# Kernel optimization log

Hardware: AMD Instinct MI355X
Metric: run time of the kernel (lower is better)

## Reference

```python
import jax, jax.numpy as jnp
import numpy as np
import math

B, H, S, D = 2, 16, 2048, 64


def setup_inputs() -> dict:
    key = jax.random.key(0)
    kq, kk, kv = jax.random.split(key, 3)
    q = jax.random.normal(kq, (B, H, S, D), dtype=jnp.float32)
    k = jax.random.normal(kk, (B, H, S, D), dtype=jnp.float32)
    v = jax.random.normal(kv, (B, H, S, D), dtype=jnp.float32)
    # causal lower-triangular mask, broadcastable to [B, H, S, S]
    mask = jnp.tril(jnp.ones((S, S), dtype=jnp.int32))[None, None, :, :]
    return {"q": q, "k": k, "v": v, "mask": mask}


def reference(q, k, v, mask):
    d_tensor = q.shape[-1]
    # scores: [B, H, S, S] = q @ k^T / sqrt(d)
    scores = jnp.einsum("bhqd,bhkd->bhqk", q, k) / math.sqrt(d_tensor)
    scores = jnp.where(mask == 0, jnp.float32(-100000.0), scores)
    attn = jax.nn.softmax(scores, axis=-1)
    out = jnp.einsum("bhqk,bhkd->bhqd", attn, v)
    return (out, attn)
```

## Files before the change

### kernel.cpp

```cpp
#include <hip/hip_runtime.h>

#define S_LEN 2048
#define D_DIM 64
#define NBH   32
#define BQ    64
#define SCALE2 0.1803368801f
#define KST   72

typedef _Float16 half8 __attribute__((ext_vector_type(8)));
typedef _Float16 half4 __attribute__((ext_vector_type(4)));
typedef float    fx4   __attribute__((ext_vector_type(4)));

#define BAR() do {                                            \
    asm volatile("s_waitcnt lgkmcnt(0)" ::: "memory");        \
    __builtin_amdgcn_s_barrier();                             \
    asm volatile("" ::: "memory");                            \
} while (0)

__global__ __launch_bounds__(256, 3)
void attn_fused(const float* __restrict__ Q, const float* __restrict__ K,
                const float* __restrict__ V, float* __restrict__ Out,
                float* __restrict__ Attn) {
    const int bh  = blockIdx.x;
    const int qt  = (int)(gridDim.y - 1) - (int)blockIdx.y;
    const int q0  = qt * BQ;
    const int T   = qt + 1;

    const int tid  = threadIdx.x;
    const int lane = tid & 63;
    const int w    = tid >> 6;
    const int ln15 = lane & 15;
    const int quad = lane >> 4;

    __shared__ _Float16 smem[5 * 64 * KST];
    _Float16 (*kb0)[KST] = (_Float16 (*)[KST])&smem[0];
    _Float16 (*kb1)[KST] = (_Float16 (*)[KST])&smem[64 * KST];
    _Float16 (*vb0)[KST] = (_Float16 (*)[KST])&smem[2 * 64 * KST];
    _Float16 (*vb1)[KST] = (_Float16 (*)[KST])&smem[3 * 64 * KST];
    _Float16 (*pw)[KST]  = (_Float16 (*)[KST])&smem[4 * 64 * KST + w * 16 * KST];
    _Float16 (*q_s)[KST] = kb1;

    const float* Qb = Q + ((size_t)bh * S_LEN + q0) * D_DIM;
    const float* Kb = K + (size_t)bh * S_LEN * D_DIM;
    const float* Vb = V + (size_t)bh * S_LEN * D_DIM;

    const int sr  = tid >> 4;
    const int sc4 = tid & 15;
    const int vc4 = tid >> 4;
    const int vjg = tid & 15;

    const float4* ks0 = (const float4*)Kb;
    float4 kf0 = ks0[tid], kf1 = ks0[256 + tid], kf2 = ks0[512 + tid], kf3 = ks0[768 + tid];
    {
        const float4* src = (const float4*)Qb;
        #pragma unroll
        for (int u = 0; u < 4; ++u) {
            int i = u * 256 + tid;
            int r = i >> 4, c4 = i & 15;
            float4 f = src[i];
            half4 h = {(_Float16)(f.x * SCALE2), (_Float16)(f.y * SCALE2),
                       (_Float16)(f.z * SCALE2), (_Float16)(f.w * SCALE2)};
            *(half4*)&q_s[r][c4 * 4] = h;
        }
    }
    __syncthreads();

    const int mrow = w * 16 + ln15;
    const half8 a_q0 = *(const half8*)&q_s[mrow][quad * 8];
    const half8 a_q1 = *(const half8*)&q_s[mrow][32 + quad * 8];

    const int qrow0 = q0 + w * 16 + quad * 4;

    float l_r[4] = {0.f, 0.f, 0.f, 0.f};

    for (int t = 0; t < T; ++t) {
        _Float16 (*kb)[KST] = (t & 1) ? kb1 : kb0;
        {
            half4 h0 = {(_Float16)kf0.x, (_Float16)kf0.y, (_Float16)kf0.z, (_Float16)kf0.w};
            half4 h1 = {(_Float16)kf1.x, (_Float16)kf1.y, (_Float16)kf1.z, (_Float16)kf1.w};
            half4 h2 = {(_Float16)kf2.x, (_Float16)kf2.y, (_Float16)kf2.z, (_Float16)kf2.w};
            half4 h3 = {(_Float16)kf3.x, (_Float16)kf3.y, (_Float16)kf3.z, (_Float16)kf3.w};
            *(half4*)&kb[sr +  0][sc4 * 4] = h0;
            *(half4*)&kb[sr + 16][sc4 * 4] = h1;
            *(half4*)&kb[sr + 32][sc4 * 4] = h2;
            *(half4*)&kb[sr + 48][sc4 * 4] = h3;
        }
        BAR();

        if (t + 1 < T) {
            const float4* kn = (const float4*)(Kb + (size_t)(t + 1) * 64 * D_DIM);
            kf0 = kn[tid]; kf1 = kn[256 + tid]; kf2 = kn[512 + tid]; kf3 = kn[768 + tid];
        }

        fx4 sC[4];
        #pragma unroll
        for (int nt = 0; nt < 4; ++nt) {
            fx4 z = {0.f, 0.f, 0.f, 0.f};
            half8 b0 = *(const half8*)&kb[nt * 16 + ln15][quad * 8];
            half8 b1 = *(const half8*)&kb[nt * 16 + ln15][32 + quad * 8];
            z = __builtin_amdgcn_mfma_f32_16x16x32_f16(a_q0, b0, z, 0, 0, 0);
            z = __builtin_amdgcn_mfma_f32_16x16x32_f16(a_q1, b1, z, 0, 0, 0);
            sC[nt] = z;
        }

        if (t < T - 1) {
            #pragma unroll
            for (int nt = 0; nt < 4; ++nt)
                #pragma unroll
                for (int r = 0; r < 4; ++r)
                    l_r[r] += exp2f(sC[nt][r]);
        } else {
            const int j0 = t * 64;
            #pragma unroll
            for (int nt = 0; nt < 4; ++nt) {
                int jc = j0 + nt * 16 + ln15;
                #pragma unroll
                for (int r = 0; r < 4; ++r) {
                    float x = (jc <= qrow0 + r) ? sC[nt][r] : -1e30f;
                    l_r[r] += exp2f(x);
                }
            }
        }
    }
    BAR();

    float inv_l[4];
    #pragma unroll
    for (int r = 0; r < 4; ++r) {
        float s = l_r[r];
        s += __shfl_xor(s, 1);
        s += __shfl_xor(s, 2);
        s += __shfl_xor(s, 4);
        s += __shfl_xor(s, 8);
        inv_l[r] = 1.0f / s;
    }

    fx4 oacc[4];
    #pragma unroll
    for (int dt = 0; dt < 4; ++dt) oacc[dt] = (fx4){0.f, 0.f, 0.f, 0.f};

    float4 vf0, vf1, vf2, vf3;
    {
        kf0 = ks0[tid]; kf1 = ks0[256 + tid]; kf2 = ks0[512 + tid]; kf3 = ks0[768 + tid];
        const float4* vs = (const float4*)Vb;
        vf0 = vs[(vjg * 4 + 0) * 16 + vc4];
        vf1 = vs[(vjg * 4 + 1) * 16 + vc4];
        vf2 = vs[(vjg * 4 + 2) * 16 + vc4];
        vf3 = vs[(vjg * 4 + 3) * 16 + vc4];
    }

    for (int t = 0; t < T; ++t) {
        const int j0 = t * 64;
        _Float16 (*kb)[KST] = (t & 1) ? kb1 : kb0;
        _Float16 (*vb)[KST] = (t & 1) ? vb1 : vb0;

        {
            half4 h0 = {(_Float16)kf0.x, (_Float16)kf0.y, (_Float16)kf0.z, (_Float16)kf0.w};
            half4 h1 = {(_Float16)kf1.x, (_Float16)kf1.y, (_Float16)kf1.z, (_Float16)kf1.w};
            half4 h2 = {(_Float16)kf2.x, (_Float16)kf2.y, (_Float16)kf2.z, (_Float16)kf2.w};
            half4 h3 = {(_Float16)kf3.x, (_Float16)kf3.y, (_Float16)kf3.z, (_Float16)kf3.w};
            *(half4*)&kb[sr +  0][sc4 * 4] = h0;
            *(half4*)&kb[sr + 16][sc4 * 4] = h1;
            *(half4*)&kb[sr + 32][sc4 * 4] = h2;
            *(half4*)&kb[sr + 48][sc4 * 4] = h3;
            half4 t0 = {(_Float16)vf0.x, (_Float16)vf1.x, (_Float16)vf2.x, (_Float16)vf3.x};
            half4 t1 = {(_Float16)vf0.y, (_Float16)vf1.y, (_Float16)vf2.y, (_Float16)vf3.y};
            half4 t2 = {(_Float16)vf0.z, (_Float16)vf1.z, (_Float16)vf2.z, (_Float16)vf3.z};
            half4 t3 = {(_Float16)vf0.w, (_Float16)vf1.w, (_Float16)vf2.w, (_Float16)vf3.w};
            *(half4*)&vb[vc4 * 4 + 0][vjg * 4] = t0;
            *(half4*)&vb[vc4 * 4 + 1][vjg * 4] = t1;
            *(half4*)&vb[vc4 * 4 + 2][vjg * 4] = t2;
            *(half4*)&vb[vc4 * 4 + 3][vjg * 4] = t3;
        }
        BAR();

        if (t + 1 < T) {
            const float4* kn = (const float4*)(Kb + (size_t)(t + 1) * 64 * D_DIM);
            kf0 = kn[tid]; kf1 = kn[256 + tid]; kf2 = kn[512 + tid]; kf3 = kn[768 + tid];
            const float4* vn = (const float4*)(Vb + (size_t)(t + 1) * 64 * D_DIM);
            vf0 = vn[(vjg * 4 + 0) * 16 + vc4];
            vf1 = vn[(vjg * 4 + 1) * 16 + vc4];
            vf2 = vn[(vjg * 4 + 2) * 16 + vc4];
            vf3 = vn[(vjg * 4 + 3) * 16 + vc4];
        }

        fx4 sC[4];
        #pragma unroll
        for (int nt = 0; nt < 4; ++nt) {
            fx4 z = {0.f, 0.f, 0.f, 0.f};
            half8 b0 = *(const half8*)&kb[nt * 16 + ln15][quad * 8];
            half8 b1 = *(const half8*)&kb[nt * 16 + ln15][32 + quad * 8];
            z = __builtin_amdgcn_mfma_f32_16x16x32_f16(a_q0, b0, z, 0, 0, 0);
            z = __builtin_amdgcn_mfma_f32_16x16x32_f16(a_q1, b1, z, 0, 0, 0);
            sC[nt] = z;
        }

        if (t < T - 1) {
            #pragma unroll
            for (int nt = 0; nt < 4; ++nt) {
                int jc = j0 + nt * 16 + ln15;
                #pragma unroll
                for (int r = 0; r < 4; ++r) {
                    float p = exp2f(sC[nt][r]) * inv_l[r];
                    Attn[((size_t)bh * S_LEN + (size_t)(qrow0 + r)) * S_LEN + jc] = p;
                    pw[quad * 4 + r][nt * 16 + ln15] = (_Float16)p;
                }
            }
        } else {
            #pragma unroll
            for (int nt = 0; nt < 4; ++nt) {
                int jc = j0 + nt * 16 + ln15;
                #pragma unroll
                for (int r = 0; r < 4; ++r) {
                    float x = (jc <= qrow0 + r) ? sC[nt][r] : -1e30f;
                    float p = exp2f(x) * inv_l[r];
                    Attn[((size_t)bh * S_LEN + (size_t)(qrow0 + r)) * S_LEN + jc] = p;
                    pw[quad * 4 + r][nt * 16 + ln15] = (_Float16)p;
                }
            }
        }

        {
            half8 a_p0 = *(const half8*)&pw[ln15][quad * 8];
            half8 a_p1 = *(const half8*)&pw[ln15][32 + quad * 8];
            #pragma unroll
            for (int dt = 0; dt < 4; ++dt) {
                half8 bv0 = *(const half8*)&vb[dt * 16 + ln15][quad * 8];
                half8 bv1 = *(const half8*)&vb[dt * 16 + ln15][32 + quad * 8];
                oacc[dt] = __builtin_amdgcn_mfma_f32_16x16x32_f16(a_p0, bv0, oacc[dt], 0, 0, 0);
                oacc[dt] = __builtin_amdgcn_mfma_f32_16x16x32_f16(a_p1, bv1, oacc[dt], 0, 0, 0);
            }
        }
    }

    #pragma unroll
    for (int dt = 0; dt < 4; ++dt) {
        #pragma unroll
        for (int r = 0; r < 4; ++r) {
            size_t oidx = ((size_t)bh * S_LEN + (size_t)(qrow0 + r)) * D_DIM + dt * 16 + ln15;
            Out[oidx] = oacc[dt][r];
        }
    }

    {
        const int jend = q0 + BQ;
        const int rowlen4 = (S_LEN - jend) >> 2;
        if (rowlen4 > 0) {
            fx4 z = {0.f, 0.f, 0.f, 0.f};
            for (int r = w; r < BQ; r += 4) {
                fx4* dst = (fx4*)(Attn + ((size_t)bh * S_LEN + (size_t)(q0 + r)) * S_LEN + jend);
                for (int c = lane; c < rowlen4; c += 64) dst[c] = z;
            }
        }
    }
}

extern "C" void kernel_launch(void* const* d_in, const int* in_sizes, int n_in,
                              void* d_out, int out_size, void* d_ws, size_t ws_size,
                              hipStream_t stream) {
    const float* q = (const float*)d_in[0];
    const float* k = (const float*)d_in[1];
    const float* v = (const float*)d_in[2];
    float* out  = (float*)d_out;
    float* attn = out + (size_t)NBH * S_LEN * D_DIM;
    dim3 grid(NBH, S_LEN / BQ);
    attn_fused<<<grid, 256, 0, stream>>>(q, k, v, out, attn);
}
```

Before: 670.6 us.

## Replace two-pass softmax with single pass plus normalization fixup of Attn rows

Removes the first pass over K that only computed row sums, and computes the softmax numerators in the single main loop while accumulating the row sum. Out is scaled by the inverse sum at the end. The unnormalized Attn entries already written to global memory are then read back, scaled and rewritten, and the masked tail is zero-filled in the same sweep. This saves one full QK^T recompute but adds a read-modify-write of the whole causal Attn region, which is large. Like the old code it subtracts no row maximum, so it relies on scores staying small enough for exp2 not to overflow.

```diff
diff --git a/kernel.cpp b/kernel.cpp
--- a/kernel.cpp
+++ b/kernel.cpp
@@ -33,6 +33,7 @@
     const int quad = lane >> 4;
 
     __shared__ _Float16 smem[5 * 64 * KST];
+    __shared__ float l_inv_s[BQ];
     _Float16 (*kb0)[KST] = (_Float16 (*)[KST])&smem[0];
     _Float16 (*kb1)[KST] = (_Float16 (*)[KST])&smem[64 * KST];
     _Float16 (*vb0)[KST] = (_Float16 (*)[KST])&smem[2 * 64 * KST];
@@ -49,8 +50,16 @@
     const int vc4 = tid >> 4;
     const int vjg = tid & 15;
 
-    const float4* ks0 = (const float4*)Kb;
-    float4 kf0 = ks0[tid], kf1 = ks0[256 + tid], kf2 = ks0[512 + tid], kf3 = ks0[768 + tid];
+    float4 kf0, kf1, kf2, kf3, vf0, vf1, vf2, vf3;
+    {
+        const float4* ks = (const float4*)Kb;
+        kf0 = ks[tid]; kf1 = ks[256 + tid]; kf2 = ks[512 + tid]; kf3 = ks[768 + tid];
+        const float4* vs = (const float4*)Vb;
+        vf0 = vs[(vjg * 4 + 0) * 16 + vc4];
+        vf1 = vs[(vjg * 4 + 1) * 16 + vc4];
+        vf2 = vs[(vjg * 4 + 2) * 16 + vc4];
+        vf3 = vs[(vjg * 4 + 3) * 16 + vc4];
+    }
     {
         const float4* src = (const float4*)Qb;
         #pragma unroll
@@ -63,7 +72,7 @@
             *(half4*)&q_s[r][c4 * 4] = h;
         }
     }
-    __syncthreads();
+    BAR();
 
     const int mrow = w * 16 + ln15;
     const half8 a_q0 = *(const half8*)&q_s[mrow][quad * 8];
@@ -72,82 +81,9 @@
     const int qrow0 = q0 + w * 16 + quad * 4;
 
     float l_r[4] = {0.f, 0.f, 0.f, 0.f};
-
-    for (int t = 0; t < T; ++t) {
-        _Float16 (*kb)[KST] = (t & 1) ? kb1 : kb0;
-        {
-            half4 h0 = {(_Float16)kf0.x, (_Float16)kf0.y, (_Float16)kf0.z, (_Float16)kf0.w};
-            half4 h1 = {(_Float16)kf1.x, (_Float16)kf1.y, (_Float16)kf1.z, (_Float16)kf1.w};
-            half4 h2 = {(_Float16)kf2.x, (_Float16)kf2.y, (_Float16)kf2.z, (_Float16)kf2.w};
-            half4 h3 = {(_Float16)kf3.x, (_Float16)kf3.y, (_Float16)kf3.z, (_Float16)kf3.w};
-            *(half4*)&kb[sr +  0][sc4 * 4] = h0;
-            *(half4*)&kb[sr + 16][sc4 * 4] = h1;
-            *(half4*)&kb[sr + 32][sc4 * 4] = h2;
-            *(half4*)&kb[sr + 48][sc4 * 4] = h3;
-        }
-        BAR();
-
-        if (t + 1 < T) {
-            const float4* kn = (const float4*)(Kb + (size_t)(t + 1) * 64 * D_DIM);
-            kf0 = kn[tid]; kf1 = kn[256 + tid]; kf2 = kn[512 + tid]; kf3 = kn[768 + tid];
-        }
-
-        fx4 sC[4];
-        #pragma unroll
-        for (int nt = 0; nt < 4; ++nt) {
-            fx4 z = {0.f, 0.f, 0.f, 0.f};
-            half8 b0 = *(const half8*)&kb[nt * 16 + ln15][quad * 8];
-            half8 b1 = *(const half8*)&kb[nt * 16 + ln15][32 + quad * 8];
-            z = __builtin_amdgcn_mfma_f32_16x16x32_f16(a_q0, b0, z, 0, 0, 0);
-            z = __builtin_amdgcn_mfma_f32_16x16x32_f16(a_q1, b1, z, 0, 0, 0);
-            sC[nt] = z;
-        }
-
-        if (t < T - 1) {
-            #pragma unroll
-            for (int nt = 0; nt < 4; ++nt)
-                #pragma unroll
-                for (int r = 0; r < 4; ++r)
-                    l_r[r] += exp2f(sC[nt][r]);
-        } else {
-            const int j0 = t * 64;
-            #pragma unroll
-            for (int nt = 0; nt < 4; ++nt) {
-                int jc = j0 + nt * 16 + ln15;
-                #pragma unroll
-                for (int r = 0; r < 4; ++r) {
-                    float x = (jc <= qrow0 + r) ? sC[nt][r] : -1e30f;
-                    l_r[r] += exp2f(x);
-                }
-            }
-        }
-    }
-    BAR();
-
-    float inv_l[4];
-    #pragma unroll
-    for (int r = 0; r < 4; ++r) {
-        float s = l_r[r];
-        s += __shfl_xor(s, 1);
-        s += __shfl_xor(s, 2);
-        s += __shfl_xor(s, 4);
-        s += __shfl_xor(s, 8);
-        inv_l[r] = 1.0f / s;
-    }
-
     fx4 oacc[4];
     #pragma unroll
     for (int dt = 0; dt < 4; ++dt) oacc[dt] = (fx4){0.f, 0.f, 0.f, 0.f};
-
-    float4 vf0, vf1, vf2, vf3;
-    {
-        kf0 = ks0[tid]; kf1 = ks0[256 + tid]; kf2 = ks0[512 + tid]; kf3 = ks0[768 + tid];
-        const float4* vs = (const float4*)Vb;
-        vf0 = vs[(vjg * 4 + 0) * 16 + vc4];
-        vf1 = vs[(vjg * 4 + 1) * 16 + vc4];
-        vf2 = vs[(vjg * 4 + 2) * 16 + vc4];
-        vf3 = vs[(vjg * 4 + 3) * 16 + vc4];
-    }
 
     for (int t = 0; t < T; ++t) {
         const int j0 = t * 64;
@@ -201,7 +137,8 @@
                 int jc = j0 + nt * 16 + ln15;
                 #pragma unroll
                 for (int r = 0; r < 4; ++r) {
-                    float p = exp2f(sC[nt][r]) * inv_l[r];
+                    float p = exp2f(sC[nt][r]);
+                    l_r[r] += p;
                     Attn[((size_t)bh * S_LEN + (size_t)(qrow0 + r)) * S_LEN + jc] = p;
                     pw[quad * 4 + r][nt * 16 + ln15] = (_Float16)p;
                 }
@@ -213,7 +150,8 @@
                 #pragma unroll
                 for (int r = 0; r < 4; ++r) {
                     float x = (jc <= qrow0 + r) ? sC[nt][r] : -1e30f;
-                    float p = exp2f(x) * inv_l[r];
+                    float p = exp2f(x);
+                    l_r[r] += p;
                     Attn[((size_t)bh * S_LEN + (size_t)(qrow0 + r)) * S_LEN + jc] = p;
                     pw[quad * 4 + r][nt * 16 + ln15] = (_Float16)p;
                 }
@@ -233,23 +171,42 @@
         }
     }
 
+    float invl[4];
+    #pragma unroll
+    for (int r = 0; r < 4; ++r) {
+        float s = l_r[r];
+        s += __shfl_xor(s, 1);
+        s += __shfl_xor(s, 2);
+        s += __shfl_xor(s, 4);
+        s += __shfl_xor(s, 8);
+        invl[r] = 1.0f / s;
+        if (ln15 == r) l_inv_s[w * 16 + quad * 4 + r] = invl[r];
+    }
     #pragma unroll
     for (int dt = 0; dt < 4; ++dt) {
         #pragma unroll
         for (int r = 0; r < 4; ++r) {
             size_t oidx = ((size_t)bh * S_LEN + (size_t)(qrow0 + r)) * D_DIM + dt * 16 + ln15;
-            Out[oidx] = oacc[dt][r];
-        }
-    }
+            Out[oidx] = oacc[dt][r] * invl[r];
+        }
+    }
+
+    __syncthreads();
 
     {
-        const int jend = q0 + BQ;
-        const int rowlen4 = (S_LEN - jend) >> 2;
-        if (rowlen4 > 0) {
-            fx4 z = {0.f, 0.f, 0.f, 0.f};
-            for (int r = w; r < BQ; r += 4) {
-                fx4* dst = (fx4*)(Attn + ((size_t)bh * S_LEN + (size_t)(q0 + r)) * S_LEN + jend);
-                for (int c = lane; c < rowlen4; c += 64) dst[c] = z;
+        const int jcut = q0 + BQ;
+        float* base = Attn + ((size_t)bh * S_LEN + (size_t)q0) * S_LEN;
+        for (int c = tid; c < BQ * (S_LEN / 4); c += 256) {
+            int row = c >> 9;
+            int j   = (c & 511) << 2;
+            float4* ptr = (float4*)(base + (size_t)row * S_LEN + j);
+            if (j < jcut) {
+                float il = l_inv_s[row];
+                float4 v = *ptr;
+                v.x *= il; v.y *= il; v.z *= il; v.w *= il;
+                *ptr = v;
+            } else {
+                *ptr = (float4){0.f, 0.f, 0.f, 0.f};
             }
         }
     }
```

New measurement: 782.9 us. 16.8% more time.

## Double query tile to 128 rows with 8 waves sharing each K/V tile

Applied to the files above, without the earlier changes.

Raises the query block to 128 rows handled by 8 waves of 512 threads, so each K/V tile staged in shared memory is reused by twice as many query rows and total K/V global traffic is halved. Per-wave causal skipping is added: waves whose rows lie entirely above a key tile skip its MMA work and write zeros to the attention matrix directly. The V transpose staging changes to half2 stores, and shared memory grows by one tile. The tradeoff is fewer blocks, coarser causal load balancing, and idle waves on diagonal tiles.

```diff
diff --git a/kernel.cpp b/kernel.cpp
--- a/kernel.cpp
+++ b/kernel.cpp
@@ -3,13 +3,14 @@
 #define S_LEN 2048
 #define D_DIM 64
 #define NBH   32
-#define BQ    64
+#define BQ    128
 #define SCALE2 0.1803368801f
 #define KST   72
 
-typedef _Float16 half8 __attribute__((ext_vector_type(8)));
-typedef _Float16 half4 __attribute__((ext_vector_type(4)));
-typedef float    fx4   __attribute__((ext_vector_type(4)));
+typedef _Float16 half8  __attribute__((ext_vector_type(8)));
+typedef _Float16 half4  __attribute__((ext_vector_type(4)));
+typedef _Float16 half2v __attribute__((ext_vector_type(2)));
+typedef float    fx4    __attribute__((ext_vector_type(4)));
 
 #define BAR() do {                                            \
     asm volatile("s_waitcnt lgkmcnt(0)" ::: "memory");        \
@@ -17,14 +18,14 @@
     asm volatile("" ::: "memory");                            \
 } while (0)
 
-__global__ __launch_bounds__(256, 3)
+__global__ __launch_bounds__(512, 4)
 void attn_fused(const float* __restrict__ Q, const float* __restrict__ K,
                 const float* __restrict__ V, float* __restrict__ Out,
                 float* __restrict__ Attn) {
     const int bh  = blockIdx.x;
     const int qt  = (int)(gridDim.y - 1) - (int)blockIdx.y;
     const int q0  = qt * BQ;
-    const int T   = qt + 1;
+    const int T   = 2 * qt + 2;
 
     const int tid  = threadIdx.x;
     const int lane = tid & 63;
@@ -32,13 +33,13 @@
     const int ln15 = lane & 15;
     const int quad = lane >> 4;
 
-    __shared__ _Float16 smem[5 * 64 * KST];
+    __shared__ _Float16 smem[6 * 64 * KST];
     _Float16 (*kb0)[KST] = (_Float16 (*)[KST])&smem[0];
     _Float16 (*kb1)[KST] = (_Float16 (*)[KST])&smem[64 * KST];
     _Float16 (*vb0)[KST] = (_Float16 (*)[KST])&smem[2 * 64 * KST];
     _Float16 (*vb1)[KST] = (_Float16 (*)[KST])&smem[3 * 64 * KST];
     _Float16 (*pw)[KST]  = (_Float16 (*)[KST])&smem[4 * 64 * KST + w * 16 * KST];
-    _Float16 (*q_s)[KST] = kb1;
+    _Float16 (*q_s)[KST] = kb0;
 
     const float* Qb = Q + ((size_t)bh * S_LEN + q0) * D_DIM;
     const float* Kb = K + (size_t)bh * S_LEN * D_DIM;
@@ -46,16 +47,16 @@
 
     const int sr  = tid >> 4;
     const int sc4 = tid & 15;
-    const int vc4 = tid >> 4;
-    const int vjg = tid & 15;
+    const int vp2 = tid & 31;
+    const int vc  = tid >> 5;
 
     const float4* ks0 = (const float4*)Kb;
-    float4 kf0 = ks0[tid], kf1 = ks0[256 + tid], kf2 = ks0[512 + tid], kf3 = ks0[768 + tid];
+    float4 kf0 = ks0[tid], kf1 = ks0[512 + tid];
     {
         const float4* src = (const float4*)Qb;
         #pragma unroll
         for (int u = 0; u < 4; ++u) {
-            int i = u * 256 + tid;
+            int i = u * 512 + tid;
             int r = i >> 4, c4 = i & 15;
             float4 f = src[i];
             half4 h = {(_Float16)(f.x * SCALE2), (_Float16)(f.y * SCALE2),
@@ -63,13 +64,15 @@
             *(half4*)&q_s[r][c4 * 4] = h;
         }
     }
-    __syncthreads();
+    BAR();
 
     const int mrow = w * 16 + ln15;
     const half8 a_q0 = *(const half8*)&q_s[mrow][quad * 8];
     const half8 a_q1 = *(const half8*)&q_s[mrow][32 + quad * 8];
-
-    const int qrow0 = q0 + w * 16 + quad * 4;
+    BAR();
+
+    const int wrow0 = q0 + w * 16;
+    const int qrow0 = wrow0 + quad * 4;
 
     float l_r[4] = {0.f, 0.f, 0.f, 0.f};
 
@@ -78,19 +81,18 @@
         {
             half4 h0 = {(_Float16)kf0.x, (_Float16)kf0.y, (_Float16)kf0.z, (_Float16)kf0.w};
             half4 h1 = {(_Float16)kf1.x, (_Float16)kf1.y, (_Float16)kf1.z, (_Float16)kf1.w};
-            half4 h2 = {(_Float16)kf2.x, (_Float16)kf2.y, (_Float16)kf2.z, (_Float16)kf2.w};
-            half4 h3 = {(_Float16)kf3.x, (_Float16)kf3.y, (_Float16)kf3.z, (_Float16)kf3.w};
             *(half4*)&kb[sr +  0][sc4 * 4] = h0;
-            *(half4*)&kb[sr + 16][sc4 * 4] = h1;
-            *(half4*)&kb[sr + 32][sc4 * 4] = h2;
-            *(half4*)&kb[sr + 48][sc4 * 4] = h3;
+            *(half4*)&kb[sr + 32][sc4 * 4] = h1;
         }
         BAR();
 
         if (t + 1 < T) {
             const float4* kn = (const float4*)(Kb + (size_t)(t + 1) * 64 * D_DIM);
-            kf0 = kn[tid]; kf1 = kn[256 + tid]; kf2 = kn[512 + tid]; kf3 = kn[768 + tid];
-        }
+            kf0 = kn[tid]; kf1 = kn[512 + tid];
+        }
+
+        const int j0 = t * 64;
+        if (j0 > wrow0 + 15) continue;
 
         fx4 sC[4];
         #pragma unroll
@@ -103,14 +105,13 @@
             sC[nt] = z;
         }
 
-        if (t < T - 1) {
+        if (j0 + 63 <= wrow0) {
             #pragma unroll
             for (int nt = 0; nt < 4; ++nt)
                 #pragma unroll
                 for (int r = 0; r < 4; ++r)
                     l_r[r] += exp2f(sC[nt][r]);
         } else {
-            const int j0 = t * 64;
             #pragma unroll
             for (int nt = 0; nt < 4; ++nt) {
                 int jc = j0 + nt * 16 + ln15;
@@ -139,14 +140,12 @@
     #pragma unroll
     for (int dt = 0; dt < 4; ++dt) oacc[dt] = (fx4){0.f, 0.f, 0.f, 0.f};
 
-    float4 vf0, vf1, vf2, vf3;
+    float4 vf0, vf1;
     {
-        kf0 = ks0[tid]; kf1 = ks0[256 + tid]; kf2 = ks0[512 + tid]; kf3 = ks0[768 + tid];
+        kf0 = ks0[tid]; kf1 = ks0[512 + tid];
         const float4* vs = (const float4*)Vb;
-        vf0 = vs[(vjg * 4 + 0) * 16 + vc4];
-        vf1 = vs[(vjg * 4 + 1) * 16 + vc4];
-        vf2 = vs[(vjg * 4 + 2) * 16 + vc4];
-        vf3 = vs[(vjg * 4 + 3) * 16 + vc4];
+        vf0 = vs[(2 * vp2 + 0) * 16 + vc];
+        vf1 = vs[(2 * vp2 + 1) * 16 + vc];
     }
 
     for (int t = 0; t < T; ++t) {
@@ -157,31 +156,33 @@
         {
             half4 h0 = {(_Float16)kf0.x, (_Float16)kf0.y, (_Float16)kf0.z, (_Float16)kf0.w};
             half4 h1 = {(_Float16)kf1.x, (_Float16)kf1.y, (_Float16)kf1.z, (_Float16)kf1.w};
-            half4 h2 = {(_Float16)kf2.x, (_Float16)kf2.y, (_Float16)kf2.z, (_Float16)kf2.w};
-            half4 h3 = {(_Float16)kf3.x, (_Float16)kf3.y, (_Float16)kf3.z, (_Float16)kf3.w};
             *(half4*)&kb[sr +  0][sc4 * 4] = h0;
-            *(half4*)&kb[sr + 16][sc4 * 4] = h1;
-            *(half4*)&kb[sr + 32][sc4 * 4] = h2;
-            *(half4*)&kb[sr + 48][sc4 * 4] = h3;
-            half4 t0 = {(_Float16)vf0.x, (_Float16)vf1.x, (_Float16)vf2.x, (_Float16)vf3.x};
-            half4 t1 = {(_Float16)vf0.y, (_Float16)vf1.y, (_Float16)vf2.y, (_Float16)vf3.y};
-            half4 t2 = {(_Float16)vf0.z, (_Float16)vf1.z, (_Float16)vf2.z, (_Float16)vf3.z};
-            half4 t3 = {(_Float16)vf0.w, (_Float16)vf1.w, (_Float16)vf2.w, (_Float16)vf3.w};
-            *(half4*)&vb[vc4 * 4 + 0][vjg * 4] = t0;
-            *(half4*)&vb[vc4 * 4 + 1][vjg * 4] = t1;
-            *(half4*)&vb[vc4 * 4 + 2][vjg * 4] = t2;
-            *(half4*)&vb[vc4 * 4 + 3][vjg * 4] = t3;
+            *(half4*)&kb[sr + 32][sc4 * 4] = h1;
+            #pragma unroll
+            for (int i = 0; i < 4; ++i) {
+                half2v h = {(_Float16)vf0[i], (_Float16)vf1[i]};
+                *(half2v*)&vb[vc * 4 + i][2 * vp2] = h;
+            }
         }
         BAR();
 
         if (t + 1 < T) {
             const float4* kn = (const float4*)(Kb + (size_t)(t + 1) * 64 * D_DIM);
-            kf0 = kn[tid]; kf1 = kn[256 + tid]; kf2 = kn[512 + tid]; kf3 = kn[768 + tid];
+            kf0 = kn[tid]; kf1 = kn[512 + tid];
             const float4* vn = (const float4*)(Vb + (size_t)(t + 1) * 64 * D_DIM);
-            vf0 = vn[(vjg * 4 + 0) * 16 + vc4];
-            vf1 = vn[(vjg * 4 + 1) * 16 + vc4];
-            vf2 = vn[(vjg * 4 + 2) * 16 + vc4];
-            vf3 = vn[(vjg * 4 + 3) * 16 + vc4];
+            vf0 = vn[(2 * vp2 + 0) * 16 + vc];
+            vf1 = vn[(2 * vp2 + 1) * 16 + vc];
+        }
+
+        if (j0 > wrow0 + 15) {
+            #pragma unroll
+            for (int nt = 0; nt < 4; ++nt) {
+                int jc = j0 + nt * 16 + ln15;
+                #pragma unroll
+                for (int r = 0; r < 4; ++r)
+                    Attn[((size_t)bh * S_LEN + (size_t)(qrow0 + r)) * S_LEN + jc] = 0.0f;
+            }
+            continue;
         }
 
         fx4 sC[4];
@@ -195,7 +196,7 @@
             sC[nt] = z;
         }
 
-        if (t < T - 1) {
+        if (j0 + 63 <= wrow0) {
             #pragma unroll
             for (int nt = 0; nt < 4; ++nt) {
                 int jc = j0 + nt * 16 + ln15;
@@ -247,7 +248,7 @@
         const int rowlen4 = (S_LEN - jend) >> 2;
         if (rowlen4 > 0) {
             fx4 z = {0.f, 0.f, 0.f, 0.f};
-            for (int r = w; r < BQ; r += 4) {
+            for (int r = w; r < BQ; r += 8) {
                 fx4* dst = (fx4*)(Attn + ((size_t)bh * S_LEN + (size_t)(q0 + r)) * S_LEN + jend);
                 for (int c = lane; c < rowlen4; c += 64) dst[c] = z;
             }
@@ -264,5 +265,5 @@
     float* out  = (float*)d_out;
     float* attn = out + (size_t)NBH * S_LEN * D_DIM;
     dim3 grid(NBH, S_LEN / BQ);
-    attn_fused<<<grid, 256, 0, stream>>>(q, k, v, out, attn);
+    attn_fused<<<grid, 512, 0, stream>>>(q, k, v, out, attn);
 }
```

Result: faster. 643.1 us (-4.1%).
